# Optimization experiments

Measured on AMD Instinct MI355X. Metric: run time of the kernel, lower is better.

Reference implementation:

```python
import jax, jax.numpy as jnp
import numpy as np

DIMS = [1024, 2048, 2048, 51]
B, P = 16, 1024


def setup_inputs() -> dict:
    key = jax.random.key(0)
    ks = jax.random.split(key, 1 + 2 * (len(DIMS) - 1))
    inp = {
        "num_pairs": P,
        "classifier_input": jax.random.normal(ks[0], (B, P, DIMS[0]), dtype=jnp.float32),
        "num_batches": B,
    }
    # Linear params, PyTorch-style: W[out, in], b[out]
    for li in range(len(DIMS) - 1):
        fan_in = DIMS[li]
        bound = 1.0 / np.sqrt(fan_in)
        inp[f"W{li}"] = jax.random.uniform(ks[1 + 2 * li], (DIMS[li + 1], fan_in), minval=-bound, maxval=bound, dtype=jnp.float32)
        inp[f"b{li}"] = jax.random.uniform(ks[2 + 2 * li], (DIMS[li + 1],), minval=-bound, maxval=bound, dtype=jnp.float32)
    return inp


def reference(num_pairs, classifier_input, num_batches, W0, b0, W1, b1, W2, b2):
    # Batched MLP over all (num_batches * num_pairs) vectors at once.
    # Original loops per (b, i); math is identical. dropout p=0.0 -> identity.
    x = classifier_input  # [B, P, d_in]
    x = jax.nn.relu(jnp.einsum("bpd,hd->bph", x, W0) + b0)
    x = jax.nn.relu(jnp.einsum("bpd,hd->bph", x, W1) + b1)
    out = jnp.einsum("bpd,od->bpo", x, W2) + b2  # [B, P, n_classes]
    return out
```

## Files before the change

### kernel.cpp

```cpp
#include <hip/hip_runtime.h>
#include <hip/hip_bf16.h>
#include <stdint.h>

typedef __attribute__((ext_vector_type(8))) short short8;
typedef __attribute__((ext_vector_type(8))) uint16_t ushort8;
typedef __attribute__((ext_vector_type(4))) float floatx4;

#define TK 64


__device__ __forceinline__ uint16_t f2bf_bits(float f) {
    uint32_t u = __builtin_bit_cast(uint32_t, f);
    u += 0x7FFFu + ((u >> 16) & 1u);
    return (uint16_t)(u >> 16);
}

__device__ __forceinline__ void async_copy16(const void* g, void* l) {
    auto gp = (const __attribute__((address_space(1))) uint32_t*)(uintptr_t)g;
    auto lp = (__attribute__((address_space(3))) uint32_t*)(uint32_t)(uintptr_t)l;
    __builtin_amdgcn_global_load_lds(gp, lp, 16, 0, 0);
}


__global__ void cvt8(const float* __restrict__ src, uint16_t* __restrict__ dst, int n) {
    int i = (blockIdx.x * 256 + threadIdx.x) * 8;
    if (i >= n) return;
    floatx4 a = *(const floatx4*)(src + i);
    floatx4 b = *(const floatx4*)(src + i + 4);
    ushort8 o;
#pragma unroll
    for (int k = 0; k < 4; k++) {
        o[k]     = f2bf_bits(a[k]);
        o[k + 4] = f2bf_bits(b[k]);
    }
    *(ushort8*)(dst + i) = o;
}

__global__ void cvt_pad_w2(const float* __restrict__ src, uint16_t* __restrict__ dst) {
    int i = (blockIdx.x * 256 + threadIdx.x) * 8;
    int row = i >> 11;
    ushort8 o;
    if (row < 51) {
        floatx4 a = *(const floatx4*)(src + i);
        floatx4 b = *(const floatx4*)(src + i + 4);
#pragma unroll
        for (int k = 0; k < 4; k++) {
            o[k]     = f2bf_bits(a[k]);
            o[k + 4] = f2bf_bits(b[k]);
        }
    } else {
#pragma unroll
        for (int k = 0; k < 8; k++) o[k] = 0;
    }
    *(ushort8*)(dst + i) = o;
}


template <int MI, int NJ, bool RELU, bool OUTF32>
__global__ __launch_bounds__(256, 2)
void gemm_bt(const uint16_t* __restrict__ A,
             const uint16_t* __restrict__ W,
             const float* __restrict__ bias,
             void* __restrict__ out,
             int M, int N, int K, int ldc, int nstore)
{
    constexpr int TMv = MI * 32;
    constexpr int TNv = NJ * 32;
    constexpr int ACH = TMv / 32;
    constexpr int BCH = TNv / 32;

    __shared__ alignas(16) uint16_t sA[TMv * TK];
    __shared__ alignas(16) uint16_t sB[TNv * TK];

    const int tid  = threadIdx.x;
    const int wave = tid >> 6;
    const int lane = tid & 63;

    const int f   = blockIdx.x;
    const int xcd = f & 7;
    const int loc = f >> 3;
    const int per = (int)gridDim.x >> 3;
    const int nt  = N / TNv;
    const int n_t = loc % nt;
    const int m_t = xcd * (per / nt) + loc / nt;
    const int n0 = n_t * TNv;
    const int m0 = m_t * TMv;

    floatx4 acc[MI][NJ];
    const floatx4 zero = {0.f, 0.f, 0.f, 0.f};
#pragma unroll
    for (int i = 0; i < MI; i++)
#pragma unroll
        for (int j = 0; j < NJ; j++) acc[i][j] = zero;

    const int wr = (wave >> 1) * MI * 16;
    const int wc = (wave & 1) * NJ * 16;

    const int sr   = lane >> 3;
    const int scol = ((lane & 7) ^ sr) * 8;

    const uint16_t* ap[ACH];
    const uint16_t* bp[BCH];
#pragma unroll
    for (int t = 0; t < ACH; t++)
        ap[t] = A + (size_t)(m0 + (wave + 4 * t) * 8 + sr) * K + scol;
#pragma unroll
    for (int t = 0; t < BCH; t++)
        bp[t] = W + (size_t)(n0 + (wave + 4 * t) * 8 + sr) * K + scol;

    const int fm = lane & 15;
    const int fr = fm & 7;
    const int kgb = lane >> 4;

    const int niter = K / TK;
    for (int it = 0; it < niter; it++) {
#pragma unroll
        for (int t = 0; t < ACH; t++) {
            async_copy16(ap[t], sA + (wave + 4 * t) * 512);
            ap[t] += TK;
        }
#pragma unroll
        for (int t = 0; t < BCH; t++) {
            async_copy16(bp[t], sB + (wave + 4 * t) * 512);
            bp[t] += TK;
        }
        __syncthreads();

#pragma unroll
        for (int kk = 0; kk < 2; kk++) {
            const int slot = ((kgb + 4 * kk) ^ fr) * 8;
            short8 af[MI], bfr[NJ];
#pragma unroll
            for (int i = 0; i < MI; i++)
                af[i] = *(const short8*)(sA + (wr + i * 16 + fm) * TK + slot);
#pragma unroll
            for (int j = 0; j < NJ; j++)
                bfr[j] = *(const short8*)(sB + (wc + j * 16 + fm) * TK + slot);
#pragma unroll
            for (int i = 0; i < MI; i++)
#pragma unroll
                for (int j = 0; j < NJ; j++)
                    acc[i][j] = __builtin_amdgcn_mfma_f32_16x16x32_bf16(af[i], bfr[j], acc[i][j], 0, 0, 0);
        }
        __syncthreads();
    }

    const int cr = (lane >> 4) * 4;
    const int cc = lane & 15;
#pragma unroll
    for (int i = 0; i < MI; i++) {
        const int gmb = m0 + wr + i * 16 + cr;
#pragma unroll
        for (int j = 0; j < NJ; j++) {
            const int gn = n0 + wc + j * 16 + cc;
            if (gn < nstore) {
                const float bv = bias[gn];
#pragma unroll
                for (int r = 0; r < 4; r++) {
                    float v = acc[i][j][r] + bv;
                    if (RELU) v = fmaxf(v, 0.f);
                    const size_t idx = (size_t)(gmb + r) * ldc + gn;
                    if (OUTF32) ((float*)out)[idx] = v;
                    else        ((uint16_t*)out)[idx] = f2bf_bits(v);
                }
            }
        }
    }
}


#define SCHED0 __builtin_amdgcn_sched_barrier(0)

#define LOAD_A(SA, QM) do { \
    const uint16_t* _p = (SA) + (QM) * 8192 + aoff; \
    _Pragma("unroll") \
    for (int kk = 0; kk < 2; kk++) { \
      const int sl = ((kgb + 4 * kk) ^ fr) * 8; \
      _Pragma("unroll") \
      for (int mi = 0; mi < 4; mi++) \
        af[mi][kk] = *(const short8*)(_p + mi * 1024 + sl); \
    } } while (0)

#define LOAD_B(SB, QN, BF) do { \
    const uint16_t* _p = (SB) + (QN) * 8192 + boff; \
    _Pragma("unroll") \
    for (int kk = 0; kk < 2; kk++) { \
      const int sl = ((kgb + 4 * kk) ^ fr) * 8; \
      _Pragma("unroll") \
      for (int nj = 0; nj < 2; nj++) \
        BF[nj][kk] = *(const short8*)(_p + nj * 1024 + sl); \
    } } while (0)

#define PH_SYNC \
    SCHED0; \
    asm volatile("s_waitcnt lgkmcnt(0)" ::: "memory"); \
    SCHED0; \
    __builtin_amdgcn_s_barrier(); \
    SCHED0;

#define PH_SYNC_CKPT(NSTR) \
    SCHED0; \
    asm volatile("s_waitcnt lgkmcnt(0)" ::: "memory"); \
    SCHED0; \
    asm volatile("s_waitcnt vmcnt(" NSTR ")" ::: "memory"); \
    SCHED0; \
    __builtin_amdgcn_s_barrier(); \
    SCHED0;

#define MFMA_CL(QM, QN, BF) \
    __builtin_amdgcn_s_setprio(1); \
    _Pragma("unroll") \
    for (int kk = 0; kk < 2; kk++) \
      _Pragma("unroll") \
      for (int mi = 0; mi < 4; mi++) \
        _Pragma("unroll") \
        for (int nj = 0; nj < 2; nj++) \
          acc[QM][QN][mi][nj] = __builtin_amdgcn_mfma_f32_16x16x32_bf16( \
              af[mi][kk], BF[nj][kk], acc[QM][QN][mi][nj], 0, 0, 0); \
    __builtin_amdgcn_s_setprio(0); \
    SCHED0;

#define ITER_BODY(T, LAST) \
     \
    LOAD_A(sA0, 0); \
    LOAD_B(sB0, 0, b0); \
    stA(1, (T) + 1, sA1); \
    PH_SYNC; \
    MFMA_CL(0, 0, b0); \
     \
    LOAD_B(sB0, 1, b1); \
    if (!(LAST)) stA(0, (T) + 2, sA0); \
    PH_SYNC; \
    MFMA_CL(0, 1, b1); \
     \
    LOAD_A(sA0, 1); \
    if (!(LAST)) stB(0, (T) + 2, sB0); \
    PH_SYNC; \
    MFMA_CL(1, 1, b1); \
     \
    if (!(LAST)) { \
      stB(1, (T) + 2, sB0); \
      PH_SYNC_CKPT("6"); \
    } else { \
      PH_SYNC_CKPT("0"); \
    } \
    MFMA_CL(1, 0, b0); \
     \
    LOAD_A(sA1, 0); \
    LOAD_B(sB1, 0, b0); \
    if (!(LAST)) stA(1, (T) + 2, sA0); \
    PH_SYNC; \
    MFMA_CL(0, 0, b0); \
     \
    LOAD_B(sB1, 1, b1); \
    if (!(LAST)) stA(0, (T) + 3, sA1); \
    PH_SYNC; \
    MFMA_CL(0, 1, b1); \
     \
    LOAD_A(sA1, 1); \
    if (!(LAST)) stB(0, (T) + 3, sB1); \
    PH_SYNC; \
    MFMA_CL(1, 1, b1); \
     \
    if (!(LAST)) { \
      stB(1, (T) + 3, sB1); \
      PH_SYNC_CKPT("6"); \
    } else { \
      PH_SYNC; \
    } \
    MFMA_CL(1, 0, b0);

template <bool RELU, bool OUTF32>
__global__ __launch_bounds__(512, 2)
void gemm256(const uint16_t* __restrict__ A,
             const uint16_t* __restrict__ W,
             const float* __restrict__ bias,
             void* __restrict__ out,
             int K, int N, int ldc, int nstore)
{
    extern __shared__ uint16_t smem[];
    uint16_t* sA0 = smem;
    uint16_t* sA1 = smem + 16384;
    uint16_t* sB0 = smem + 32768;
    uint16_t* sB1 = smem + 49152;

    const int tid  = threadIdx.x;
    const int wave = tid >> 6;
    const int lane = tid & 63;
    const int wm2  = wave >> 2;
    const int wn2  = wave & 3;

    const int f   = blockIdx.x;
    const int xcd = f & 7;
    const int loc = f >> 3;
    const int per = (int)gridDim.x >> 3;
    const int ntn = N / 256;
    const int n_t = loc % ntn;
    const int m_t = xcd * (per / ntn) + loc / ntn;
    const int m0 = m_t * 256;
    const int n0 = n_t * 256;

    floatx4 acc[2][2][4][2];
    const floatx4 zero = {0.f, 0.f, 0.f, 0.f};
#pragma unroll
    for (int qm = 0; qm < 2; qm++)
#pragma unroll
    for (int qn = 0; qn < 2; qn++)
#pragma unroll
    for (int mi = 0; mi < 4; mi++)
#pragma unroll
    for (int nj = 0; nj < 2; nj++) acc[qm][qn][mi][nj] = zero;

    const int srow = lane >> 3;
    const int scol = ((lane & 7) ^ srow) * 8;
    const uint16_t* pA = A + (size_t)(m0 + wave * 8 + srow) * K + scol;
    const uint16_t* pB = W + (size_t)(n0 + wave * 8 + srow) * K + scol;

    auto stA = [&](int h, int kt, uint16_t* buf) {
        const uint16_t* p = pA + (size_t)h * 128 * K + (size_t)kt * 64;
        async_copy16(p,                  buf + h * 8192 + wave * 512);
        async_copy16(p + (size_t)64 * K, buf + h * 8192 + 4096 + wave * 512);
    };
    auto stB = [&](int h, int kt, uint16_t* buf) {
        const uint16_t* p = pB + (size_t)h * 128 * K + (size_t)kt * 64;
        async_copy16(p,                  buf + h * 8192 + wave * 512);
        async_copy16(p + (size_t)64 * K, buf + h * 8192 + 4096 + wave * 512);
    };

    const int fm  = lane & 15;
    const int fr  = fm & 7;
    const int kgb = lane >> 4;
    const int aoff = (wm2 * 64 + fm) * 64;
    const int boff = (wn2 * 32 + fm) * 64;

    short8 af[4][2];
    short8 b0[2][2];
    short8 b1[2][2];

    stA(0, 0, sA0);
    stB(0, 0, sB0);
    stA(1, 0, sA0);
    stB(1, 0, sB0);
    stA(0, 1, sA1);
    stB(0, 1, sB1);
    stB(1, 1, sB1);
    asm volatile("s_waitcnt vmcnt(6)" ::: "memory");
    __builtin_amdgcn_s_barrier();
    SCHED0;

    const int niter2 = K / 128;
    for (int it = 0; it < niter2 - 1; ++it) {
        const int T = 2 * it;
        ITER_BODY(T, false);
    }
    {
        const int T = 2 * (niter2 - 1);
        ITER_BODY(T, true);
    }

    const int cr = (lane >> 4) * 4;
    const int cc = lane & 15;
#pragma unroll
    for (int qm = 0; qm < 2; qm++)
#pragma unroll
    for (int mi = 0; mi < 4; mi++) {
        const int gm = m0 + qm * 128 + wm2 * 64 + mi * 16 + cr;
#pragma unroll
        for (int qn = 0; qn < 2; qn++)
#pragma unroll
        for (int nj = 0; nj < 2; nj++) {
            const int gn = n0 + qn * 128 + wn2 * 32 + nj * 16 + cc;
            if (gn < nstore) {
                const float bv = bias[gn];
#pragma unroll
                for (int r = 0; r < 4; r++) {
                    float v = acc[qm][qn][mi][nj][r] + bv;
                    if (RELU) v = fmaxf(v, 0.f);
                    const size_t idx = (size_t)(gm + r) * ldc + gn;
                    if (OUTF32) ((float*)out)[idx] = v;
                    else        ((uint16_t*)out)[idx] = f2bf_bits(v);
                }
            }
        }
    }
}


extern "C" void kernel_launch(void* const* d_in, const int* in_sizes, int n_in,
                              void* d_out, int out_size, void* d_ws, size_t ws_size,
                              hipStream_t stream) {
    (void)in_sizes; (void)n_in; (void)out_size; (void)ws_size;
    const float* X  = (const float*)d_in[1];
    const float* W0 = (const float*)d_in[3];
    const float* b0 = (const float*)d_in[4];
    const float* W1 = (const float*)d_in[5];
    const float* b1 = (const float*)d_in[6];
    const float* W2 = (const float*)d_in[7];
    const float* b2 = (const float*)d_in[8];

    const int M = 16384;

    static bool attr_done = false;
    if (!attr_done) {
        (void)hipFuncSetAttribute((const void*)gemm256<true, false>,
                                  hipFuncAttributeMaxDynamicSharedMemorySize, 131072);
        attr_done = true;
    }

    char* w = (char*)d_ws;
    uint16_t* X0  = (uint16_t*)w; w += (size_t)M * 1024 * 2;
    uint16_t* X1  = (uint16_t*)w; w += (size_t)M * 2048 * 2;
    uint16_t* X2  = (uint16_t*)w; w += (size_t)M * 2048 * 2;
    uint16_t* W0b = (uint16_t*)w; w += (size_t)2048 * 1024 * 2;
    uint16_t* W1b = (uint16_t*)w; w += (size_t)2048 * 2048 * 2;
    uint16_t* W2b = (uint16_t*)w; w += (size_t)64 * 2048 * 2;

    cvt8<<<M * 1024 / 8 / 256, 256, 0, stream>>>(X, X0, M * 1024);
    cvt8<<<2048 * 1024 / 8 / 256, 256, 0, stream>>>(W0, W0b, 2048 * 1024);
    cvt8<<<2048 * 2048 / 8 / 256, 256, 0, stream>>>(W1, W1b, 2048 * 2048);
    cvt_pad_w2<<<64 * 2048 / 8 / 256, 256, 0, stream>>>(W2, W2b);

    gemm256<true, false><<<dim3((M / 256) * (2048 / 256)), 512, 131072, stream>>>(
        X0, W0b, b0, X1, 1024, 2048, 2048, 2048);
    gemm256<true, false><<<dim3((M / 256) * (2048 / 256)), 512, 131072, stream>>>(
        X1, W1b, b1, X2, 2048, 2048, 2048, 2048);
    gemm_bt<1, 2, false, true><<<dim3(M / 32), 256, 0, stream>>>(
        X2, W2b, b2, d_out, M, 64, 2048, 51, 51);
}
```

Measured before the change: 347.7 us.

## Fuse conversion kernels into one launch and add direct-load small-N final GEMM

Replaces the four separate fp32-to-bf16 conversion launches with a single grid-stride kernel covering X and all three weights, padding W2 with zeros. Replaces the LDS-staged final GEMM (N=64) with a kernel that loads A and W fragments straight from global memory into MFMA operands, removing shared-memory staging and barriers. The goal is fewer launches and less synchronization overhead. In exchange, the conversion kernel has more branching per element, and the direct global loads are less coalesced (16-byte strided rows) and each wave-pair rereads W2.

Result: slower. 362.7 us (+4.3%).

```diff
diff --git a/kernel.cpp b/kernel.cpp
--- a/kernel.cpp
+++ b/kernel.cpp
@@ -5,8 +5,6 @@
 typedef __attribute__((ext_vector_type(8))) short short8;
 typedef __attribute__((ext_vector_type(8))) uint16_t ushort8;
 typedef __attribute__((ext_vector_type(4))) float floatx4;
-
-#define TK 64
 
 
 __device__ __forceinline__ uint16_t f2bf_bits(float f) {
@@ -22,147 +20,100 @@
 }
 
 
-__global__ void cvt8(const float* __restrict__ src, uint16_t* __restrict__ dst, int n) {
-    int i = (blockIdx.x * 256 + threadIdx.x) * 8;
-    if (i >= n) return;
-    floatx4 a = *(const floatx4*)(src + i);
-    floatx4 b = *(const floatx4*)(src + i + 4);
-    ushort8 o;
-#pragma unroll
-    for (int k = 0; k < 4; k++) {
-        o[k]     = f2bf_bits(a[k]);
-        o[k + 4] = f2bf_bits(b[k]);
-    }
-    *(ushort8*)(dst + i) = o;
-}
-
-__global__ void cvt_pad_w2(const float* __restrict__ src, uint16_t* __restrict__ dst) {
-    int i = (blockIdx.x * 256 + threadIdx.x) * 8;
-    int row = i >> 11;
-    ushort8 o;
-    if (row < 51) {
-        floatx4 a = *(const floatx4*)(src + i);
-        floatx4 b = *(const floatx4*)(src + i + 4);
-#pragma unroll
-        for (int k = 0; k < 4; k++) {
-            o[k]     = f2bf_bits(a[k]);
-            o[k + 4] = f2bf_bits(b[k]);
-        }
-    } else {
-#pragma unroll
-        for (int k = 0; k < 8; k++) o[k] = 0;
-    }
-    *(ushort8*)(dst + i) = o;
-}
-
-
-template <int MI, int NJ, bool RELU, bool OUTF32>
-__global__ __launch_bounds__(256, 2)
-void gemm_bt(const uint16_t* __restrict__ A,
-             const uint16_t* __restrict__ W,
-             const float* __restrict__ bias,
-             void* __restrict__ out,
-             int M, int N, int K, int ldc, int nstore)
+__global__ void cvt_all(const float* __restrict__ X,  const float* __restrict__ W0,
+                        const float* __restrict__ W1, const float* __restrict__ W2,
+                        uint16_t* __restrict__ X0,  uint16_t* __restrict__ W0b,
+                        uint16_t* __restrict__ W1b, uint16_t* __restrict__ W2b) {
+    constexpr int NX  = 16384 * 1024 / 8;
+    constexpr int NW0 = 2048 * 1024 / 8;
+    constexpr int NW1 = 2048 * 2048 / 8;
+    constexpr int NW2 = 64 * 2048 / 8;
+    constexpr int TOT = NX + NW0 + NW1 + NW2;
+
+    for (int i = blockIdx.x * 256 + threadIdx.x; i < TOT; i += gridDim.x * 256) {
+        const float* src;
+        uint16_t* dst;
+        int j;
+        bool zero = false;
+        if (i < NX)                    { src = X;  dst = X0;  j = i; }
+        else if (i < NX + NW0)         { src = W0; dst = W0b; j = i - NX; }
+        else if (i < NX + NW0 + NW1)   { src = W1; dst = W1b; j = i - NX - NW0; }
+        else {
+            j = i - NX - NW0 - NW1; src = W2; dst = W2b;
+            zero = (j >> 8) >= 51;
+        }
+        ushort8 o;
+        if (!zero) {
+            floatx4 a = *(const floatx4*)(src + (size_t)j * 8);
+            floatx4 b = *(const floatx4*)(src + (size_t)j * 8 + 4);
+#pragma unroll
+            for (int k = 0; k < 4; k++) {
+                o[k]     = f2bf_bits(a[k]);
+                o[k + 4] = f2bf_bits(b[k]);
+            }
+        } else {
+#pragma unroll
+            for (int k = 0; k < 8; k++) o[k] = 0;
+        }
+        *(ushort8*)(dst + (size_t)j * 8) = o;
+    }
+}
+
+
+template <bool RELU, bool OUTF32>
+__global__ __launch_bounds__(256)
+void gemm_small_n(const uint16_t* __restrict__ A,
+                  const uint16_t* __restrict__ W,
+                  const float* __restrict__ bias,
+                  void* __restrict__ out,
+                  int K, int ldc, int nstore)
 {
-    constexpr int TMv = MI * 32;
-    constexpr int TNv = NJ * 32;
-    constexpr int ACH = TMv / 32;
-    constexpr int BCH = TNv / 32;
-
-    __shared__ alignas(16) uint16_t sA[TMv * TK];
-    __shared__ alignas(16) uint16_t sB[TNv * TK];
-
     const int tid  = threadIdx.x;
     const int wave = tid >> 6;
     const int lane = tid & 63;
-
-    const int f   = blockIdx.x;
-    const int xcd = f & 7;
-    const int loc = f >> 3;
-    const int per = (int)gridDim.x >> 3;
-    const int nt  = N / TNv;
-    const int n_t = loc % nt;
-    const int m_t = xcd * (per / nt) + loc / nt;
-    const int n0 = n_t * TNv;
-    const int m0 = m_t * TMv;
-
-    floatx4 acc[MI][NJ];
-    const floatx4 zero = {0.f, 0.f, 0.f, 0.f};
-#pragma unroll
-    for (int i = 0; i < MI; i++)
-#pragma unroll
-        for (int j = 0; j < NJ; j++) acc[i][j] = zero;
-
-    const int wr = (wave >> 1) * MI * 16;
-    const int wc = (wave & 1) * NJ * 16;
-
-    const int sr   = lane >> 3;
-    const int scol = ((lane & 7) ^ sr) * 8;
-
-    const uint16_t* ap[ACH];
-    const uint16_t* bp[BCH];
-#pragma unroll
-    for (int t = 0; t < ACH; t++)
-        ap[t] = A + (size_t)(m0 + (wave + 4 * t) * 8 + sr) * K + scol;
-#pragma unroll
-    for (int t = 0; t < BCH; t++)
-        bp[t] = W + (size_t)(n0 + (wave + 4 * t) * 8 + sr) * K + scol;
-
-    const int fm = lane & 15;
-    const int fr = fm & 7;
+    const int wr = (wave >> 1) * 16;
+    const int wc = (wave & 1) * 32;
+
+    const int m0 = blockIdx.x * 32;
+    const int fm  = lane & 15;
     const int kgb = lane >> 4;
 
-    const int niter = K / TK;
-    for (int it = 0; it < niter; it++) {
-#pragma unroll
-        for (int t = 0; t < ACH; t++) {
-            async_copy16(ap[t], sA + (wave + 4 * t) * 512);
-            ap[t] += TK;
-        }
-#pragma unroll
-        for (int t = 0; t < BCH; t++) {
-            async_copy16(bp[t], sB + (wave + 4 * t) * 512);
-            bp[t] += TK;
-        }
-        __syncthreads();
-
+    const uint16_t* pa  = A + (size_t)(m0 + wr + fm) * K + kgb * 8;
+    const uint16_t* pb0 = W + (size_t)(wc + fm) * K + kgb * 8;
+    const uint16_t* pb1 = W + (size_t)(wc + 16 + fm) * K + kgb * 8;
+
+    floatx4 acc0 = {0.f, 0.f, 0.f, 0.f};
+    floatx4 acc1 = {0.f, 0.f, 0.f, 0.f};
+
+#pragma unroll 8
+    for (int k0 = 0; k0 < K; k0 += 64) {
 #pragma unroll
         for (int kk = 0; kk < 2; kk++) {
-            const int slot = ((kgb + 4 * kk) ^ fr) * 8;
-            short8 af[MI], bfr[NJ];
-#pragma unroll
-            for (int i = 0; i < MI; i++)
-                af[i] = *(const short8*)(sA + (wr + i * 16 + fm) * TK + slot);
-#pragma unroll
-            for (int j = 0; j < NJ; j++)
-                bfr[j] = *(const short8*)(sB + (wc + j * 16 + fm) * TK + slot);
-#pragma unroll
-            for (int i = 0; i < MI; i++)
-#pragma unroll
-                for (int j = 0; j < NJ; j++)
-                    acc[i][j] = __builtin_amdgcn_mfma_f32_16x16x32_bf16(af[i], bfr[j], acc[i][j], 0, 0, 0);
-        }
-        __syncthreads();
+            const int off = k0 + kk * 32;
+            short8 a  = *(const short8*)(pa  + off);
+            short8 b0 = *(const short8*)(pb0 + off);
+            short8 b1 = *(const short8*)(pb1 + off);
+            acc0 = __builtin_amdgcn_mfma_f32_16x16x32_bf16(a, b0, acc0, 0, 0, 0);
+            acc1 = __builtin_amdgcn_mfma_f32_16x16x32_bf16(a, b1, acc1, 0, 0, 0);
+        }
     }
 
     const int cr = (lane >> 4) * 4;
     const int cc = lane & 15;
-#pragma unroll
-    for (int i = 0; i < MI; i++) {
-        const int gmb = m0 + wr + i * 16 + cr;
-#pragma unroll
-        for (int j = 0; j < NJ; j++) {
-            const int gn = n0 + wc + j * 16 + cc;
-            if (gn < nstore) {
-                const float bv = bias[gn];
-#pragma unroll
-                for (int r = 0; r < 4; r++) {
-                    float v = acc[i][j][r] + bv;
-                    if (RELU) v = fmaxf(v, 0.f);
-                    const size_t idx = (size_t)(gmb + r) * ldc + gn;
-                    if (OUTF32) ((float*)out)[idx] = v;
-                    else        ((uint16_t*)out)[idx] = f2bf_bits(v);
-                }
+    const int gm = m0 + wr + cr;
+#pragma unroll
+    for (int j = 0; j < 2; j++) {
+        const int gn = wc + j * 16 + cc;
+        if (gn < nstore) {
+            const float bv = bias[gn];
+            const floatx4 av = j ? acc1 : acc0;
+#pragma unroll
+            for (int r = 0; r < 4; r++) {
+                float v = av[r] + bv;
+                if (RELU) v = fmaxf(v, 0.f);
+                const size_t idx = (size_t)(gm + r) * ldc + gn;
+                if (OUTF32) ((float*)out)[idx] = v;
+                else        ((uint16_t*)out)[idx] = f2bf_bits(v);
             }
         }
     }
@@ -415,15 +366,12 @@
     uint16_t* W1b = (uint16_t*)w; w += (size_t)2048 * 2048 * 2;
     uint16_t* W2b = (uint16_t*)w; w += (size_t)64 * 2048 * 2;
 
-    cvt8<<<M * 1024 / 8 / 256, 256, 0, stream>>>(X, X0, M * 1024);
-    cvt8<<<2048 * 1024 / 8 / 256, 256, 0, stream>>>(W0, W0b, 2048 * 1024);
-    cvt8<<<2048 * 2048 / 8 / 256, 256, 0, stream>>>(W1, W1b, 2048 * 2048);
-    cvt_pad_w2<<<64 * 2048 / 8 / 256, 256, 0, stream>>>(W2, W2b);
+    cvt_all<<<1024, 256, 0, stream>>>(X, W0, W1, W2, X0, W0b, W1b, W2b);
 
     gemm256<true, false><<<dim3((M / 256) * (2048 / 256)), 512, 131072, stream>>>(
         X0, W0b, b0, X1, 1024, 2048, 2048, 2048);
     gemm256<true, false><<<dim3((M / 256) * (2048 / 256)), 512, 131072, stream>>>(
         X1, W1b, b1, X2, 2048, 2048, 2048, 2048);
-    gemm_bt<1, 2, false, true><<<dim3(M / 32), 256, 0, stream>>>(
-        X2, W2b, b2, d_out, M, 64, 2048, 51, 51);
-}
+    gemm_small_n<false, true><<<dim3(M / 32), 256, 0, stream>>>(
+        X2, W2b, b2, d_out, 2048, 51, 51);
+}
```
